# Performance work log

Measured on AMD Instinct MI355X. Metric: run time of the kernel, lower is better.

The kernel has to match this reference:

```python
import jax, jax.numpy as jnp
import numpy as np

ALPHA = 0.2          # LeakyReLU negative slope
NEG_BIG = -9e15      # mask value from original code


def setup_inputs() -> dict:
    key = jax.random.key(0)
    k1, k2, k3, k4 = jax.random.split(key, 4)
    B, N, F_in, F_out = 16, 1024, 256, 256
    x = jax.random.normal(k1, (B, N, F_in), dtype=jnp.float32)
    adj = jax.random.randint(k2, (B, N, N), 0, 2, dtype=jnp.int32)
    # xavier-uniform-like scales
    W = jax.random.normal(k3, (F_in, F_out), dtype=jnp.float32) * np.sqrt(2.0 / (F_in + F_out))
    a = jax.random.normal(k4, (2 * F_out, 1), dtype=jnp.float32) * np.sqrt(2.0 / (2 * F_out + 1))
    return {"x": x, "adj": adj, "W": W, "a": a}


def reference(x, adj, W, a):
    # x: [B,N,Fin], adj: [B,N,N] (int mask), W: [Fin,Fout], a: [2*Fout,1]
    F_out = a.shape[0] // 2
    h = jnp.einsum("bni,io->bno", x, W)            # [B,N,Fout]
    # Decompose a into left/right halves: e_ij = lrelu(a_l.h_i + a_r.h_j)
    a_l = a[:F_out, 0]                               # [Fout]
    a_r = a[F_out:, 0]                               # [Fout]
    el = h @ a_l                                     # [B,N] score contribution of target i
    er = h @ a_r                                     # [B,N] score contribution of source j
    e = jax.nn.leaky_relu(el[:, :, None] + er[:, None, :], ALPHA)  # [B,N,N]
    e = jnp.where(adj > 0, e, NEG_BIG)
    attn = jax.nn.softmax(e, axis=-1)                # masked softmax over neighbors j
    # weighted sum of neighbor features; concat with n_heads=1 is identity
    return jnp.einsum("bij,bjo->bio", attn, h)       # [B,N,Fout]
```

## Files before the change

kernel.cpp:

```cpp
#include <hip/hip_runtime.h>
#include <stdint.h>

#define ALPHA 0.2f

typedef __attribute__((ext_vector_type(8))) short bf16x8;
typedef __attribute__((ext_vector_type(8))) unsigned short u16x8;
typedef __attribute__((ext_vector_type(4))) float f32x4;

__device__ __forceinline__ unsigned short f2bf(float f) {
    unsigned int u = __float_as_uint(f);
    u += 0x7fffu + ((u >> 16) & 1u);
    return (unsigned short)(u >> 16);
}

__device__ __forceinline__ void gload_lds16(const void* g, void* l) {
    __builtin_amdgcn_global_load_lds(
        (const __attribute__((address_space(1))) unsigned int*)g,
        (__attribute__((address_space(3))) unsigned int*)l, 16, 0, 0);
}

__global__ void wt_wa_kernel(const float* __restrict__ W,
                             const float* __restrict__ a,
                             unsigned short* __restrict__ Wtbf,
                             float* __restrict__ wa) {
    const int t = threadIdx.x;
    if (blockIdx.x < 256) {
        const int o = blockIdx.x;
        Wtbf[o * 256 + t] = f2bf(W[t * 256 + o]);
    } else {
        float sl = 0.f, sr = 0.f;
        const float* wr = W + t * 256;
        for (int o = 0; o < 256; ++o) {
            const float wv = wr[o];
            sl += wv * a[o];
            sr += wv * a[256 + o];
        }
        wa[t] = sl;
        wa[256 + t] = sr;
    }
}

__global__ __launch_bounds__(256) void eler2x_kernel(
    const float* __restrict__ x, const float* __restrict__ wa,
    float* __restrict__ el, float* __restrict__ er,
    unsigned short* __restrict__ xbf)
{
    const int w = threadIdx.x >> 6, l = threadIdx.x & 63;
    const int r = blockIdx.x * 4 + w;
    const float4 xv = *(const float4*)(x + (size_t)r * 256 + l * 4);
    const float4 al = *(const float4*)(wa + l * 4);
    const float4 ar = *(const float4*)(wa + 256 + l * 4);

    ushort4 xb;
    xb.x = f2bf(xv.x); xb.y = f2bf(xv.y); xb.z = f2bf(xv.z); xb.w = f2bf(xv.w);
    *(ushort4*)(xbf + (size_t)r * 256 + l * 4) = xb;

    float sl = xv.x * al.x + xv.y * al.y + xv.z * al.z + xv.w * al.w;
    float sr = xv.x * ar.x + xv.y * ar.y + xv.z * ar.z + xv.w * ar.w;
#pragma unroll
    for (int off = 32; off >= 1; off >>= 1) {
        sl += __shfl_xor(sl, off);
        sr += __shfl_xor(sr, off);
    }
    if (l == 0) { el[r] = sl; er[r] = sr; }
}

__global__ __launch_bounds__(256) void gemm_h(
    const unsigned short* __restrict__ A,
    const unsigned short* __restrict__ Bt,
    unsigned short* __restrict__ C)
{
    __shared__ __align__(16) unsigned short As[64 * 64];
    __shared__ __align__(16) unsigned short Bs[128 * 64];

    const int tid = threadIdx.x;
    const int w = tid >> 6, l = tid & 63;
    const int q = l >> 4, ml = l & 15;
    const int wm = (w >> 1) * 32;
    const int wn = (w & 1) * 64;
    const int m0 = blockIdx.y * 64;
    const int n0 = blockIdx.x * 128;

    f32x4 acc[2][4];
    for (int i = 0; i < 2; ++i)
        for (int j = 0; j < 4; ++j) {
            f32x4 z = {0.f, 0.f, 0.f, 0.f};
            acc[i][j] = z;
        }

    for (int k0 = 0; k0 < 256; k0 += 64) {
        for (int c = 0; c < 2; ++c) {
            const int cb = c * 256 + (w << 6);
            const int p = cb + l;
            const int r = p >> 3;
            const int cc = (p & 7) ^ (r & 7);
            gload_lds16(A + (size_t)(m0 + r) * 256 + k0 + cc * 8, As + cb * 8);
        }
        for (int c = 0; c < 4; ++c) {
            const int cb = c * 256 + (w << 6);
            const int p = cb + l;
            const int r = p >> 3;
            const int cc = (p & 7) ^ (r & 7);
            gload_lds16(Bt + (size_t)(n0 + r) * 256 + k0 + cc * 8, Bs + cb * 8);
        }
        __syncthreads();

        bf16x8 aF[2][2], bF[2][4];
#pragma unroll
        for (int ks = 0; ks < 2; ++ks) {
#pragma unroll
            for (int mt = 0; mt < 2; ++mt) {
                const int mm = wm + mt * 16 + ml;
                aF[ks][mt] = *(const bf16x8*)(As + (mm * 8 + ((ks * 4 + q) ^ (mm & 7))) * 8);
            }
#pragma unroll
            for (int nt = 0; nt < 4; ++nt) {
                const int nn = wn + nt * 16 + ml;
                bF[ks][nt] = *(const bf16x8*)(Bs + (nn * 8 + ((ks * 4 + q) ^ (nn & 7))) * 8);
            }
        }
#pragma unroll
        for (int ks = 0; ks < 2; ++ks)
            for (int mt = 0; mt < 2; ++mt)
                for (int nt = 0; nt < 4; ++nt)
                    acc[mt][nt] = __builtin_amdgcn_mfma_f32_16x16x32_bf16(
                        aF[ks][mt], bF[ks][nt], acc[mt][nt], 0, 0, 0);
        __syncthreads();
    }

    for (int mt = 0; mt < 2; ++mt)
        for (int nt = 0; nt < 4; ++nt) {
            const int gn = n0 + wn + nt * 16 + ml;
            for (int r = 0; r < 4; ++r) {
                const int gm = m0 + wm + mt * 16 + q * 4 + r;
                C[(size_t)gm * 16384 + gn] = f2bf(acc[mt][nt][r]);
            }
        }
}

__global__ __launch_bounds__(256) void mask_kernel(
    const int* __restrict__ adj,
    const float* __restrict__ el,
    const float* __restrict__ er,
    float* __restrict__ c,
    unsigned short* __restrict__ pk16)
{
    __shared__ unsigned char nibs[4][256];

    const int w = threadIdx.x >> 6, l = threadIdx.x & 63;
    const int row = blockIdx.x * 4 + w;
    const int b = row >> 10;
    const int* arow = adj + (size_t)row * 1024;
    const float* erb = er + (b << 10);
    const float eli = el[row];

    int4 av[4]; float4 erv[4];
#pragma unroll
    for (int it = 0; it < 4; ++it) {
        const int j = it * 256 + l * 4;
        av[it]  = *(const int4*)(arow + j);
        erv[it] = *(const float4*)(erb + j);
    }

    const float NINF = -__builtin_inff();
    float s = 0.f;
#pragma unroll
    for (int it = 0; it < 4; ++it) {
        float e0 = eli + erv[it].x; e0 = e0 > 0.f ? e0 : ALPHA * e0;
        float e1 = eli + erv[it].y; e1 = e1 > 0.f ? e1 : ALPHA * e1;
        float e2 = eli + erv[it].z; e2 = e2 > 0.f ? e2 : ALPHA * e2;
        float e3 = eli + erv[it].w; e3 = e3 > 0.f ? e3 : ALPHA * e3;
        e0 = av[it].x > 0 ? e0 : NINF;
        e1 = av[it].y > 0 ? e1 : NINF;
        e2 = av[it].z > 0 ? e2 : NINF;
        e3 = av[it].w > 0 ? e3 : NINF;
        s += __expf(e0) + __expf(e1) + __expf(e2) + __expf(e3);
        nibs[w][it * 64 + l] =
            (unsigned char)((av[it].x > 0) | ((av[it].y > 0) << 1) |
                            ((av[it].z > 0) << 2) | ((av[it].w > 0) << 3));
    }
#pragma unroll
    for (int off = 32; off >= 1; off >>= 1) s += __shfl_xor(s, off);
    if (l == 0) c[row] = __logf(s);

    const unsigned nr = *(const unsigned int*)(&nibs[w][l * 4]);
    const unsigned short mask16 =
        (unsigned short)((nr & 0xFu) | ((nr >> 4) & 0xF0u) |
                         ((nr >> 8) & 0xF00u) | ((nr >> 12) & 0xF000u));
    pk16[(size_t)row * 64 + l] = mask16;
}

__global__ __launch_bounds__(256) void pv_kernel(
    const unsigned short* __restrict__ pk16,
    const float* __restrict__ el,
    const float* __restrict__ er,
    const float* __restrict__ c,
    const unsigned short* __restrict__ hT,
    float* __restrict__ out)
{
    __shared__ float er_s[1024];
    __shared__ __align__(16) unsigned short pk_s[32 * 64];
    __shared__ __align__(16) unsigned short Hs[256 * 64];
    __shared__ __align__(16) unsigned short Ps[32 * 72];

    const int tid = threadIdx.x;
    const int w = tid >> 6, l = tid & 63;
    const int q = l >> 4, ml = l & 15;
    const int b = blockIdx.y;
    const int i0 = blockIdx.x * 32;

    *(float4*)(er_s + tid * 4) = *(const float4*)(er + (b << 10) + tid * 4);
    *(u16x8*)(pk_s + tid * 8) =
        *(const u16x8*)(pk16 + ((size_t)(b << 10) + i0) * 64 + tid * 8);
    const int ib = tid >> 3;
    const int js = (tid & 7) * 8;
    const float eli_b = el[(b << 10) + i0 + ib];
    const float ci = c[(b << 10) + i0 + ib];
    __syncthreads();

    f32x4 acc[2][4];
    for (int i = 0; i < 2; ++i)
        for (int j = 0; j < 4; ++j) {
            f32x4 z = {0.f, 0.f, 0.f, 0.f};
            acc[i][j] = z;
        }

    const unsigned short* hb = hT + (size_t)b * 1024;

    for (int j0 = 0; j0 < 1024; j0 += 64) {
        for (int cr = 0; cr < 8; ++cr) {
            const int cb = cr * 256 + (w << 6);
            const int p = cb + l;
            const int r = p >> 3;
            const int cc = (p & 7) ^ (r & 7);
            gload_lds16(hb + (size_t)r * 16384 + j0 + cc * 8, Hs + cb * 8);
        }
        {
            const unsigned hw = pk_s[ib * 64 + ((j0 + js) >> 4)];
            const unsigned v = (hw >> ((j0 + js) & 15)) & 0xFFu;
            u16x8 pvv;
#pragma unroll
            for (int u = 0; u < 8; ++u) {
                float e = eli_b + er_s[j0 + js + u];
                e = e > 0.f ? e : ALPHA * e;
                const float p = ((v >> u) & 1u) ? __expf(e - ci) : 0.f;
                pvv[u] = f2bf(p);
            }
            *(u16x8*)(Ps + ib * 72 + js) = pvv;
        }
        __syncthreads();

        bf16x8 aF[2][2], bF[2][4];
#pragma unroll
        for (int ks = 0; ks < 2; ++ks) {
#pragma unroll
            for (int mt = 0; mt < 2; ++mt)
                aF[ks][mt] = *(const bf16x8*)(Ps + (mt * 16 + ml) * 72 + ks * 32 + q * 8);
#pragma unroll
            for (int nt = 0; nt < 4; ++nt) {
                const int oc = (w << 6) + nt * 16 + ml;
                bF[ks][nt] = *(const bf16x8*)(Hs + (oc * 8 + ((ks * 4 + q) ^ (oc & 7))) * 8);
            }
        }
#pragma unroll
        for (int ks = 0; ks < 2; ++ks)
            for (int mt = 0; mt < 2; ++mt)
                for (int nt = 0; nt < 4; ++nt)
                    acc[mt][nt] = __builtin_amdgcn_mfma_f32_16x16x32_bf16(
                        aF[ks][mt], bF[ks][nt], acc[mt][nt], 0, 0, 0);
        __syncthreads();
    }

    float* ob = out + (size_t)b * 262144;
    for (int mt = 0; mt < 2; ++mt)
        for (int nt = 0; nt < 4; ++nt) {
            const int gn = (w << 6) + nt * 16 + ml;
            for (int r = 0; r < 4; ++r) {
                const int gm = i0 + mt * 16 + q * 4 + r;
                ob[(size_t)gm * 256 + gn] = acc[mt][nt][r];
            }
        }
}

extern "C" void kernel_launch(void* const* d_in, const int* in_sizes, int n_in,
                              void* d_out, int out_size, void* d_ws, size_t ws_size,
                              hipStream_t stream) {
    const float* x   = (const float*)d_in[0];
    const int*   adj = (const int*)d_in[1];
    const float* W   = (const float*)d_in[2];
    const float* a   = (const float*)d_in[3];
    float* out = (float*)d_out;

    char* ws = (char*)d_ws;
    unsigned short* Wtbf  = (unsigned short*)(ws);
    float* wa             = (float*)(ws + 131072);
    unsigned short* xbf   = (unsigned short*)(ws + 133120);
    unsigned short* h_T   = (unsigned short*)(ws + 8521728);
    float* el             = (float*)(ws + 16910336);
    float* er             = (float*)(ws + 16975872);
    float* c              = (float*)(ws + 17041408);
    unsigned short* pk16  = (unsigned short*)(ws + 17106944);

    wt_wa_kernel<<<dim3(257), dim3(256), 0, stream>>>(W, a, Wtbf, wa);

    eler2x_kernel<<<dim3(4096), dim3(256), 0, stream>>>(x, wa, el, er, xbf);

    gemm_h<<<dim3(128, 4), dim3(256), 0, stream>>>(Wtbf, xbf, h_T);

    mask_kernel<<<dim3(4096), dim3(256), 0, stream>>>(adj, el, er, c, pk16);

    pv_kernel<<<dim3(32, 16), dim3(256), 0, stream>>>(pk16, el, er, c, h_T, out);
}
```

Before: 155.4 us.

## Fuse x conversion and el/er into GEMM, fuse mask pass into PV kernel

```diff
diff --git a/kernel.cpp b/kernel.cpp
--- a/kernel.cpp
+++ b/kernel.cpp
@@ -40,38 +40,15 @@
     }
 }
 
-__global__ __launch_bounds__(256) void eler2x_kernel(
-    const float* __restrict__ x, const float* __restrict__ wa,
-    float* __restrict__ el, float* __restrict__ er,
-    unsigned short* __restrict__ xbf)
+__global__ __launch_bounds__(256) void gemm_hx(
+    const unsigned short* __restrict__ Wtbf,
+    const float* __restrict__ x,
+    const float* __restrict__ wa,
+    unsigned short* __restrict__ hT,
+    float* __restrict__ el, float* __restrict__ er)
 {
-    const int w = threadIdx.x >> 6, l = threadIdx.x & 63;
-    const int r = blockIdx.x * 4 + w;
-    const float4 xv = *(const float4*)(x + (size_t)r * 256 + l * 4);
-    const float4 al = *(const float4*)(wa + l * 4);
-    const float4 ar = *(const float4*)(wa + 256 + l * 4);
-
-    ushort4 xb;
-    xb.x = f2bf(xv.x); xb.y = f2bf(xv.y); xb.z = f2bf(xv.z); xb.w = f2bf(xv.w);
-    *(ushort4*)(xbf + (size_t)r * 256 + l * 4) = xb;
-
-    float sl = xv.x * al.x + xv.y * al.y + xv.z * al.z + xv.w * al.w;
-    float sr = xv.x * ar.x + xv.y * ar.y + xv.z * ar.z + xv.w * ar.w;
-#pragma unroll
-    for (int off = 32; off >= 1; off >>= 1) {
-        sl += __shfl_xor(sl, off);
-        sr += __shfl_xor(sr, off);
-    }
-    if (l == 0) { el[r] = sl; er[r] = sr; }
-}
-
-__global__ __launch_bounds__(256) void gemm_h(
-    const unsigned short* __restrict__ A,
-    const unsigned short* __restrict__ Bt,
-    unsigned short* __restrict__ C)
-{
-    __shared__ __align__(16) unsigned short As[64 * 64];
-    __shared__ __align__(16) unsigned short Bs[128 * 64];
+    __shared__ __align__(16) unsigned short As[64 * 256];
+    __shared__ float wa_s[512];
 
     const int tid = threadIdx.x;
     const int w = tid >> 6, l = tid & 63;
@@ -81,42 +58,60 @@
     const int m0 = blockIdx.y * 64;
     const int n0 = blockIdx.x * 128;
 
+    if (tid < 128) *(float4*)(wa_s + tid * 4) = *(const float4*)(wa + tid * 4);
+
+    for (int rd = 0; rd < 8; ++rd) {
+        const int cb = rd * 256 + (w << 6);
+        const int p = cb + l;
+        const int r = p >> 5;
+        const int c = p & 31;
+        gload_lds16(Wtbf + (size_t)(m0 + r) * 256 + ((c ^ (r & 7)) << 3),
+                    As + cb * 8);
+    }
+    __syncthreads();
+
+    const bool do_e = (blockIdx.y == 0) && (w < 2);
+
     f32x4 acc[2][4];
     for (int i = 0; i < 2; ++i)
         for (int j = 0; j < 4; ++j) {
             f32x4 z = {0.f, 0.f, 0.f, 0.f};
             acc[i][j] = z;
         }
+    float sl[4] = {0.f, 0.f, 0.f, 0.f};
+    float sr[4] = {0.f, 0.f, 0.f, 0.f};
 
     for (int k0 = 0; k0 < 256; k0 += 64) {
-        for (int c = 0; c < 2; ++c) {
-            const int cb = c * 256 + (w << 6);
-            const int p = cb + l;
-            const int r = p >> 3;
-            const int cc = (p & 7) ^ (r & 7);
-            gload_lds16(A + (size_t)(m0 + r) * 256 + k0 + cc * 8, As + cb * 8);
-        }
-        for (int c = 0; c < 4; ++c) {
-            const int cb = c * 256 + (w << 6);
-            const int p = cb + l;
-            const int r = p >> 3;
-            const int cc = (p & 7) ^ (r & 7);
-            gload_lds16(Bt + (size_t)(n0 + r) * 256 + k0 + cc * 8, Bs + cb * 8);
-        }
-        __syncthreads();
-
         bf16x8 aF[2][2], bF[2][4];
 #pragma unroll
         for (int ks = 0; ks < 2; ++ks) {
+            const int kb = k0 + ks * 32 + q * 8;
 #pragma unroll
             for (int mt = 0; mt < 2; ++mt) {
-                const int mm = wm + mt * 16 + ml;
-                aF[ks][mt] = *(const bf16x8*)(As + (mm * 8 + ((ks * 4 + q) ^ (mm & 7))) * 8);
+                const int row = wm + mt * 16 + ml;
+                const int cf = (kb >> 3) ^ (row & 7);
+                aF[ks][mt] = *(const bf16x8*)(As + (row * 32 + cf) * 8);
             }
 #pragma unroll
             for (int nt = 0; nt < 4; ++nt) {
-                const int nn = wn + nt * 16 + ml;
-                bF[ks][nt] = *(const bf16x8*)(Bs + (nn * 8 + ((ks * 4 + q) ^ (nn & 7))) * 8);
+                const int grow = n0 + wn + nt * 16 + ml;
+                const float* xp = x + (size_t)grow * 256 + kb;
+                const float4 v0 = *(const float4*)(xp);
+                const float4 v1 = *(const float4*)(xp + 4);
+                bf16x8 f;
+                f[0] = (short)f2bf(v0.x); f[1] = (short)f2bf(v0.y);
+                f[2] = (short)f2bf(v0.z); f[3] = (short)f2bf(v0.w);
+                f[4] = (short)f2bf(v1.x); f[5] = (short)f2bf(v1.y);
+                f[6] = (short)f2bf(v1.z); f[7] = (short)f2bf(v1.w);
+                bF[ks][nt] = f;
+                if (do_e) {
+                    const float* wl = wa_s + kb;
+                    const float* wrr = wa_s + 256 + kb;
+                    sl[nt] += v0.x * wl[0] + v0.y * wl[1] + v0.z * wl[2] + v0.w * wl[3]
+                            + v1.x * wl[4] + v1.y * wl[5] + v1.z * wl[6] + v1.w * wl[7];
+                    sr[nt] += v0.x * wrr[0] + v0.y * wrr[1] + v0.z * wrr[2] + v0.w * wrr[3]
+                            + v1.x * wrr[4] + v1.y * wrr[5] + v1.z * wrr[6] + v1.w * wrr[7];
+                }
             }
         }
 #pragma unroll
@@ -125,7 +120,22 @@
                 for (int nt = 0; nt < 4; ++nt)
                     acc[mt][nt] = __builtin_amdgcn_mfma_f32_16x16x32_bf16(
                         aF[ks][mt], bF[ks][nt], acc[mt][nt], 0, 0, 0);
-        __syncthreads();
+    }
+
+    if (do_e) {
+#pragma unroll
+        for (int nt = 0; nt < 4; ++nt) {
+            sl[nt] += __shfl_xor(sl[nt], 16); sl[nt] += __shfl_xor(sl[nt], 32);
+            sr[nt] += __shfl_xor(sr[nt], 16); sr[nt] += __shfl_xor(sr[nt], 32);
+        }
+        if (l < 16) {
+#pragma unroll
+            for (int nt = 0; nt < 4; ++nt) {
+                const int n = n0 + wn + nt * 16 + l;
+                el[n] = sl[nt];
+                er[n] = sr[nt];
+            }
+        }
     }
 
     for (int mt = 0; mt < 2; ++mt)
@@ -133,75 +143,27 @@
             const int gn = n0 + wn + nt * 16 + ml;
             for (int r = 0; r < 4; ++r) {
                 const int gm = m0 + wm + mt * 16 + q * 4 + r;
-                C[(size_t)gm * 16384 + gn] = f2bf(acc[mt][nt][r]);
-            }
-        }
-}
-
-__global__ __launch_bounds__(256) void mask_kernel(
+                hT[(size_t)gm * 16384 + gn] = f2bf(acc[mt][nt][r]);
+            }
+        }
+}
+
+__global__ __launch_bounds__(256) void pv_fused(
     const int* __restrict__ adj,
     const float* __restrict__ el,
     const float* __restrict__ er,
-    float* __restrict__ c,
-    unsigned short* __restrict__ pk16)
-{
-    __shared__ unsigned char nibs[4][256];
-
-    const int w = threadIdx.x >> 6, l = threadIdx.x & 63;
-    const int row = blockIdx.x * 4 + w;
-    const int b = row >> 10;
-    const int* arow = adj + (size_t)row * 1024;
-    const float* erb = er + (b << 10);
-    const float eli = el[row];
-
-    int4 av[4]; float4 erv[4];
-#pragma unroll
-    for (int it = 0; it < 4; ++it) {
-        const int j = it * 256 + l * 4;
-        av[it]  = *(const int4*)(arow + j);
-        erv[it] = *(const float4*)(erb + j);
-    }
-
-    const float NINF = -__builtin_inff();
-    float s = 0.f;
-#pragma unroll
-    for (int it = 0; it < 4; ++it) {
-        float e0 = eli + erv[it].x; e0 = e0 > 0.f ? e0 : ALPHA * e0;
-        float e1 = eli + erv[it].y; e1 = e1 > 0.f ? e1 : ALPHA * e1;
-        float e2 = eli + erv[it].z; e2 = e2 > 0.f ? e2 : ALPHA * e2;
-        float e3 = eli + erv[it].w; e3 = e3 > 0.f ? e3 : ALPHA * e3;
-        e0 = av[it].x > 0 ? e0 : NINF;
-        e1 = av[it].y > 0 ? e1 : NINF;
-        e2 = av[it].z > 0 ? e2 : NINF;
-        e3 = av[it].w > 0 ? e3 : NINF;
-        s += __expf(e0) + __expf(e1) + __expf(e2) + __expf(e3);
-        nibs[w][it * 64 + l] =
-            (unsigned char)((av[it].x > 0) | ((av[it].y > 0) << 1) |
-                            ((av[it].z > 0) << 2) | ((av[it].w > 0) << 3));
-    }
-#pragma unroll
-    for (int off = 32; off >= 1; off >>= 1) s += __shfl_xor(s, off);
-    if (l == 0) c[row] = __logf(s);
-
-    const unsigned nr = *(const unsigned int*)(&nibs[w][l * 4]);
-    const unsigned short mask16 =
-        (unsigned short)((nr & 0xFu) | ((nr >> 4) & 0xF0u) |
-                         ((nr >> 8) & 0xF00u) | ((nr >> 12) & 0xF000u));
-    pk16[(size_t)row * 64 + l] = mask16;
-}
-
-__global__ __launch_bounds__(256) void pv_kernel(
-    const unsigned short* __restrict__ pk16,
-    const float* __restrict__ el,
-    const float* __restrict__ er,
-    const float* __restrict__ c,
     const unsigned short* __restrict__ hT,
     float* __restrict__ out)
 {
     __shared__ float er_s[1024];
+    __shared__ float el_s[32];
+    __shared__ float c_s[32];
     __shared__ __align__(16) unsigned short pk_s[32 * 64];
+    __shared__ __align__(16) unsigned char buf[8192];
     __shared__ __align__(16) unsigned short Hs[256 * 64];
-    __shared__ __align__(16) unsigned short Ps[32 * 72];
+
+    unsigned char (*nibs)[256] = (unsigned char (*)[256])buf;
+    unsigned short* Ps = (unsigned short*)buf;
 
     const int tid = threadIdx.x;
     const int w = tid >> 6, l = tid & 63;
@@ -210,13 +172,56 @@
     const int i0 = blockIdx.x * 32;
 
     *(float4*)(er_s + tid * 4) = *(const float4*)(er + (b << 10) + tid * 4);
-    *(u16x8*)(pk_s + tid * 8) =
-        *(const u16x8*)(pk16 + ((size_t)(b << 10) + i0) * 64 + tid * 8);
+    if (tid < 32) el_s[tid] = el[(b << 10) + i0 + tid];
+    __syncthreads();
+
+    const float NINF = -__builtin_inff();
+    const float* erb = er + (b << 10);
+    for (int rr = 0; rr < 8; ++rr) {
+        const int row = w * 8 + rr;
+        const int* arow = adj + (size_t)((b << 10) + i0 + row) * 1024;
+        const float eli = el_s[row];
+
+        int4 av[4]; float4 erv[4];
+#pragma unroll
+        for (int it = 0; it < 4; ++it) {
+            const int j = it * 256 + l * 4;
+            av[it]  = *(const int4*)(arow + j);
+            erv[it] = *(const float4*)(erb + j);
+        }
+        float s = 0.f;
+#pragma unroll
+        for (int it = 0; it < 4; ++it) {
+            float e0 = eli + erv[it].x; e0 = e0 > 0.f ? e0 : ALPHA * e0;
+            float e1 = eli + erv[it].y; e1 = e1 > 0.f ? e1 : ALPHA * e1;
+            float e2 = eli + erv[it].z; e2 = e2 > 0.f ? e2 : ALPHA * e2;
+            float e3 = eli + erv[it].w; e3 = e3 > 0.f ? e3 : ALPHA * e3;
+            e0 = av[it].x > 0 ? e0 : NINF;
+            e1 = av[it].y > 0 ? e1 : NINF;
+            e2 = av[it].z > 0 ? e2 : NINF;
+            e3 = av[it].w > 0 ? e3 : NINF;
+            s += __expf(e0) + __expf(e1) + __expf(e2) + __expf(e3);
+            nibs[row][it * 64 + l] =
+                (unsigned char)((av[it].x > 0) | ((av[it].y > 0) << 1) |
+                                ((av[it].z > 0) << 2) | ((av[it].w > 0) << 3));
+        }
+#pragma unroll
+        for (int off = 32; off >= 1; off >>= 1) s += __shfl_xor(s, off);
+        if (l == 0) c_s[row] = __logf(s);
+    }
+    for (int rr = 0; rr < 8; ++rr) {
+        const int row = w * 8 + rr;
+        const unsigned nr = *(const unsigned int*)(&nibs[row][l * 4]);
+        pk_s[row * 64 + l] =
+            (unsigned short)((nr & 0xFu) | ((nr >> 4) & 0xF0u) |
+                             ((nr >> 8) & 0xF00u) | ((nr >> 12) & 0xF000u));
+    }
+    __syncthreads();
+
     const int ib = tid >> 3;
     const int js = (tid & 7) * 8;
-    const float eli_b = el[(b << 10) + i0 + ib];
-    const float ci = c[(b << 10) + i0 + ib];
-    __syncthreads();
+    const float eli_b = el_s[ib];
+    const float ci = c_s[ib];
 
     f32x4 acc[2][4];
     for (int i = 0; i < 2; ++i)
@@ -292,22 +297,15 @@
     float* out = (float*)d_out;
 
     char* ws = (char*)d_ws;
-    unsigned short* Wtbf  = (unsigned short*)(ws);
-    float* wa             = (float*)(ws + 131072);
-    unsigned short* xbf   = (unsigned short*)(ws + 133120);
-    unsigned short* h_T   = (unsigned short*)(ws + 8521728);
-    float* el             = (float*)(ws + 16910336);
-    float* er             = (float*)(ws + 16975872);
-    float* c              = (float*)(ws + 17041408);
-    unsigned short* pk16  = (unsigned short*)(ws + 17106944);
+    unsigned short* Wtbf = (unsigned short*)(ws);
+    float* wa            = (float*)(ws + 131072);
+    unsigned short* h_T  = (unsigned short*)(ws + 133120);
+    float* el            = (float*)(ws + 8521728);
+    float* er            = (float*)(ws + 8587264);
 
     wt_wa_kernel<<<dim3(257), dim3(256), 0, stream>>>(W, a, Wtbf, wa);
 
-    eler2x_kernel<<<dim3(4096), dim3(256), 0, stream>>>(x, wa, el, er, xbf);
-
-    gemm_h<<<dim3(128, 4), dim3(256), 0, stream>>>(Wtbf, xbf, h_T);
-
-    mask_kernel<<<dim3(4096), dim3(256), 0, stream>>>(adj, el, er, c, pk16);
-
-    pv_kernel<<<dim3(32, 16), dim3(256), 0, stream>>>(pk16, el, er, c, h_T, out);
-}
+    gemm_hx<<<dim3(128, 4), dim3(256), 0, stream>>>(Wtbf, x, wa, h_T, el, er);
+
+    pv_fused<<<dim3(32, 16), dim3(256), 0, stream>>>(adj, el, er, h_T, out);
+}
```

After: 163.2 us. 1.05x slower.
